# Optimization experiments

Measured on AMD Instinct MI355X. Metric: run time of the kernel, lower is better.

The kernel has to match this reference:

```python
import jax, jax.numpy as jnp
import numpy as np

B, H, L, DK, DV = 8, 8, 1024, 64, 64
N = B * H
TEMP = 8.0  # sqrt(d_k)
A_MIX, B_MIX, C_MIX = 0.1, 0.4, 0.1


def setup_inputs() -> dict:
    key = jax.random.key(0)
    ks = jax.random.split(key, 6)
    q = jax.random.normal(ks[0], (N, L, DK), jnp.float32)
    k = jax.random.normal(ks[1], (N, L, DK), jnp.float32)
    v = jax.random.normal(ks[2], (N, L, DV), jnp.float32)
    q_rm = jax.random.normal(ks[3], (N, L, DK), jnp.float32)
    attn_pre = jax.random.normal(ks[4], (N, L, L), jnp.float32)
    conv_w = jax.random.normal(ks[5], (H, H, 3, 3), jnp.float32) * 0.05  # OIHW, no bias
    # causal mask: True where masked (j > i), broadcast over N
    mask = jnp.broadcast_to(jnp.triu(jnp.ones((L, L), bool), 1), (N, L, L))
    return {"q": q, "k": k, "v": v, "q_rm": q_rm, "attn_pre": attn_pre,
            "conv_w": conv_w, "mask": mask, "fg": 1}


def sift_down_right(src, filled):
    # R[..,1:,1:] = src[..,:-1,:-1]; R[..,0,:] = filled[..,0,:]; R[..,:,0] = filled[..,:,0]
    top = filled[:, 0:1, :]                    # [N,1,L]
    left = filled[:, 1:, 0:1]                  # [N,L-1,1]
    body = jnp.concatenate([left, src[:, :-1, :-1]], axis=-1)  # [N,L-1,L]
    return jnp.concatenate([top, body], axis=1)


def sift_down(src, filled):
    top = filled[:, 0:1, :]
    return jnp.concatenate([top, src[:, :-1, :]], axis=1)


def reference(q, k, v, q_rm, attn_pre, conv_w, mask, fg):
    attn = jnp.einsum('nqd,nkd->nqk', q, k) / TEMP
    attn_rm = jnp.einsum('nqd,nkd->nqk', q_rm, k) / TEMP
    # conv refinement of masked attn_rm, per (batch, head) grid
    x = jnp.where(mask, 0.0, attn_rm).reshape(-1, H, L, L)  # [B,H,L,L]
    x = jax.lax.conv_general_dilated(x, conv_w, (1, 1), 'SAME',
                                     dimension_numbers=('NCHW', 'OIHW', 'NCHW'))
    x = jax.nn.relu(x).reshape(-1, L, L)
    attn_cnn = sift_down_right(x, attn_rm) if fg == 1 else sift_down(x, attn_rm)
    attn_cnn = attn_cnn * C_MIX + attn_rm * (1.0 - C_MIX)
    attn = attn_cnn * B_MIX + attn * (1.0 - B_MIX)
    attn = attn_pre * A_MIX + attn * (1.0 - A_MIX)
    attn = jnp.where(mask, -jnp.inf, attn)
    attn = jax.nn.softmax(attn, axis=-1)
    # dropout is identity in eval/deterministic baseline
    out = jnp.einsum('nqk,nkd->nqd', attn, v)
    return out, attn
```

## Files before the change

### kernel.cpp

```cpp
#include <hip/hip_runtime.h>
#include <cstdint>
#include <cstddef>
#include <math.h>

#define L_ 1024
#define DK_ 64
#define DV_ 64
#define N_ 64
#define H_ 8
#define B_ 8

__device__ __forceinline__ float bcast(float v, int src) {
  return __int_as_float(__builtin_amdgcn_readlane(__float_as_int(v), src));
}

__global__ __launch_bounds__(256) void k1_qk_tril(
    const float* __restrict__ qrm, const float* __restrict__ kk,
    float* __restrict__ xm) {
  const int n  = blockIdx.z;
  const int q0 = blockIdx.y * 64;
  const int j0 = blockIdx.x * 64;
  const int t  = threadIdx.x;

  if (j0 > q0) {
    const float4 z = make_float4(0.f, 0.f, 0.f, 0.f);
    #pragma unroll
    for (int i = 0; i < 4; ++i) {
      const int row = (t >> 4) + i * 16;
      const int c4  = t & 15;
      float4* p = (float4*)(xm + ((size_t)(n * L_ + q0 + row)) * L_ + j0);
      p[c4] = z;
    }
    return;
  }

  __shared__ float As[64][65];
  __shared__ float Bs[64][65];
  #pragma unroll
  for (int i = 0; i < 4; ++i) {
    const int row = (t >> 4) + i * 16;
    const int c4  = t & 15;
    const float4 a = ((const float4*)(qrm + ((size_t)(n * L_ + q0 + row)) * DK_))[c4];
    const float4 b = ((const float4*)(kk  + ((size_t)(n * L_ + j0 + row)) * DK_))[c4];
    As[row][c4 * 4 + 0] = a.x; As[row][c4 * 4 + 1] = a.y;
    As[row][c4 * 4 + 2] = a.z; As[row][c4 * 4 + 3] = a.w;
    Bs[row][c4 * 4 + 0] = b.x; Bs[row][c4 * 4 + 1] = b.y;
    Bs[row][c4 * 4 + 2] = b.z; Bs[row][c4 * 4 + 3] = b.w;
  }
  __syncthreads();

  const int ty = t >> 4, tx = t & 15;
  float acc[4][4];
  #pragma unroll
  for (int i = 0; i < 4; ++i)
    #pragma unroll
    for (int j = 0; j < 4; ++j) acc[i][j] = 0.f;

  for (int d = 0; d < 64; ++d) {
    float a[4], b[4];
    #pragma unroll
    for (int i = 0; i < 4; ++i) a[i] = As[ty * 4 + i][d];
    #pragma unroll
    for (int j = 0; j < 4; ++j) b[j] = Bs[tx * 4 + j][d];
    #pragma unroll
    for (int i = 0; i < 4; ++i)
      #pragma unroll
      for (int j = 0; j < 4; ++j) acc[i][j] += a[i] * b[j];
  }

  #pragma unroll
  for (int i = 0; i < 4; ++i) {
    const int gq = q0 + ty * 4 + i;
    float* rowp = xm + ((size_t)(n * L_ + gq)) * L_;
    #pragma unroll
    for (int j = 0; j < 4; ++j) {
      const int gj = j0 + tx * 4 + j;
      rowp[gj] = (gj <= gq) ? acc[i][j] * 0.125f : 0.f;
    }
  }
}

__global__ __launch_bounds__(256) void k2_conv(
    const float* __restrict__ xm, const float* __restrict__ w,
    float* __restrict__ xs) {
  const int ct = blockIdx.x, rt = blockIdx.y, b = blockIdx.z;
  const int r0 = rt * 4, c0 = ct * 64;
  if (c0 > r0 + 4) return;

  __shared__ float in_s[8][6][68];
  __shared__ float ws[576];
  const int t = threadIdx.x;

  for (int i = t; i < 576; i += 256) ws[i] = w[i];
  for (int e = t; e < 8 * 6 * 66; e += 256) {
    const int hi  = e / 396;
    const int rem = e - hi * 396;
    const int rr  = rem / 66;
    const int cc  = rem - rr * 66;
    const int gr  = r0 - 1 + rr;
    const int gc  = c0 - 1 + cc;
    float v = 0.f;
    if (gr >= 0 && gr < L_ && gc >= 0 && gc < L_)
      v = xm[((size_t)((b * 8 + hi) * L_ + gr)) * L_ + gc];
    in_s[hi][rr][cc] = v;
  }
  __syncthreads();

  const int cc = t & 63;
  const int rr = t >> 6;
  float acc[8];
  #pragma unroll
  for (int ho = 0; ho < 8; ++ho) acc[ho] = 0.f;

  #pragma unroll
  for (int hi = 0; hi < 8; ++hi) {
    float iv[3][3];
    #pragma unroll
    for (int di = 0; di < 3; ++di)
      #pragma unroll
      for (int dj = 0; dj < 3; ++dj)
        iv[di][dj] = in_s[hi][rr + di][cc + dj];
    #pragma unroll
    for (int ho = 0; ho < 8; ++ho) {
      const float* wp = &ws[(ho * 8 + hi) * 9];
      #pragma unroll
      for (int di = 0; di < 3; ++di)
        #pragma unroll
        for (int dj = 0; dj < 3; ++dj)
          acc[ho] += iv[di][dj] * wp[di * 3 + dj];
    }
  }

  const int gr = r0 + rr, gc = c0 + cc;
  #pragma unroll
  for (int ho = 0; ho < 8; ++ho)
    xs[((size_t)((b * 8 + ho) * L_ + gr)) * L_ + gc] = fmaxf(acc[ho], 0.f);
}

__global__ __launch_bounds__(256) void k3_fused(
    const float* __restrict__ q, const float* __restrict__ kk,
    const float* __restrict__ v, const float* __restrict__ pre,
    const int* __restrict__ fgp, const float* __restrict__ xs,
    float* attn, float* __restrict__ out) {
  const int bid  = blockIdx.y * gridDim.x + blockIdx.x;
  const int work = (bid & 7) * 512 + (bid >> 3);
  const int n    = work >> 6;
  const int q0   = (63 - (work & 63)) * 16;

  const int t    = threadIdx.x;
  const int lane = t & 63;
  const int g    = t >> 6;
  const int fg   = *fgp;

  const int srow = t >> 4;
  const int c4   = t & 15;

  __shared__ float tb[2][64][65];

  const float* qb = q + ((size_t)(n * L_ + q0)) * DK_;
  float qreg[4];
  #pragma unroll
  for (int i = 0; i < 4; ++i) qreg[i] = qb[(size_t)(g + i * 4) * DK_ + lane];

  float m[4], l[4];
  #pragma unroll
  for (int i = 0; i < 4; ++i) { m[i] = -INFINITY; l[i] = 0.f; }

  int r_[4];
  #pragma unroll
  for (int i = 0; i < 4; ++i) r_[i] = q0 + g + i * 4;

  const int ntiles = (q0 >> 6) + 1;
  const float* kbase = kk + (size_t)n * L_ * DK_;

  #pragma unroll
  for (int i = 0; i < 4; ++i) {
    const int row = srow + i * 16;
    const float4 kx = *(const float4*)(kbase + (size_t)row * DK_ + c4 * 4);
    tb[0][c4 * 4 + 0][row] = kx.x;
    tb[0][c4 * 4 + 1][row] = kx.y;
    tb[0][c4 * 4 + 2][row] = kx.z;
    tb[0][c4 * 4 + 3][row] = kx.w;
  }
  __syncthreads();

  for (int tile = 0; tile < ntiles; ++tile) {
    const int cur = tile & 1, nxt = cur ^ 1;
    const int j0 = tile * 64;
    const int j  = j0 + lane;
    const bool havenext = (tile + 1) < ntiles;

    float4 kpre[4];
    if (havenext) {
      const float* kb2 = kbase + (size_t)(j0 + 64) * DK_;
      #pragma unroll
      for (int i = 0; i < 4; ++i)
        kpre[i] = *(const float4*)(kb2 + (size_t)(srow + i * 16) * DK_ + c4 * 4);
    }

    float rmv[4], prv[4], xsv[4];
    #pragma unroll
    for (int i = 0; i < 4; ++i) {
      const int r = r_[i];
      const bool act = (j <= r);
      rmv[i] = act ? attn[((size_t)(n * L_ + r)) * L_ + j] : 0.f;
      prv[i] = act ? pre[((size_t)(n * L_ + r)) * L_ + j] : 0.f;
      if (fg == 1)
        xsv[i] = (act && r > 0 && j > 0)
                     ? xs[((size_t)(n * L_ + r - 1)) * L_ + (j - 1)] : 0.f;
      else
        xsv[i] = (act && r > 0)
                     ? xs[((size_t)(n * L_ + r - 1)) * L_ + j] : 0.f;
    }

    float dot[4] = {0.f, 0.f, 0.f, 0.f};
    #pragma unroll
    for (int d = 0; d < 64; ++d) {
      const float kd = tb[cur][d][lane];
      #pragma unroll
      for (int i = 0; i < 4; ++i) dot[i] += bcast(qreg[i], d) * kd;
    }

    #pragma unroll
    for (int i = 0; i < 4; ++i) {
      const int r = r_[i];
      float s = -INFINITY;
      if (j <= r) {
        const float sqk = dot[i] * 0.125f;
        const float cnn = (fg == 1)
                              ? ((r == 0 || j == 0) ? rmv[i] : xsv[i])
                              : ((r == 0) ? rmv[i] : xsv[i]);
        const float mixed = cnn * 0.1f + rmv[i] * 0.9f;
        const float a2    = mixed * 0.4f + sqk * 0.6f;
        s = prv[i] * 0.1f + a2 * 0.9f;
      }
      attn[((size_t)(n * L_ + r)) * L_ + j] = s;

      float mt = s;
      #pragma unroll
      for (int o = 32; o > 0; o >>= 1) mt = fmaxf(mt, __shfl_xor(mt, o));
      const float mn = fmaxf(m[i], mt);
      float es = __expf(s - mn);
      #pragma unroll
      for (int o = 32; o > 0; o >>= 1) es += __shfl_xor(es, o);
      l[i] = l[i] * __expf(m[i] - mn) + es;
      m[i] = mn;
    }

    if (havenext) {
      #pragma unroll
      for (int i = 0; i < 4; ++i) {
        const int row = srow + i * 16;
        tb[nxt][c4 * 4 + 0][row] = kpre[i].x;
        tb[nxt][c4 * 4 + 1][row] = kpre[i].y;
        tb[nxt][c4 * 4 + 2][row] = kpre[i].z;
        tb[nxt][c4 * 4 + 3][row] = kpre[i].w;
      }
    }
    __syncthreads();
  }

  float invl[4];
  #pragma unroll
  for (int i = 0; i < 4; ++i) invl[i] = 1.f / l[i];

  float acc[4] = {0.f, 0.f, 0.f, 0.f};
  const float* vb = v + (size_t)n * L_ * DV_;

  #pragma unroll
  for (int i = 0; i < 4; ++i) {
    const int row = srow + i * 16;
    const float4 vx = *(const float4*)(vb + (size_t)row * DV_ + c4 * 4);
    tb[0][row][c4 * 4 + 0] = vx.x;
    tb[0][row][c4 * 4 + 1] = vx.y;
    tb[0][row][c4 * 4 + 2] = vx.z;
    tb[0][row][c4 * 4 + 3] = vx.w;
  }
  float s_cur[4];
  #pragma unroll
  for (int i = 0; i < 4; ++i)
    s_cur[i] = attn[((size_t)(n * L_ + r_[i])) * L_ + lane];
  __syncthreads();

  for (int tile = 0; tile < ntiles; ++tile) {
    const int cur = tile & 1, nxt = cur ^ 1;
    const int j0 = tile * 64;
    const int j  = j0 + lane;
    const bool havenext = (tile + 1) < ntiles;

    float4 vpre[4];
    float s_nxt[4];
    if (havenext) {
      const float* vb2 = vb + (size_t)(j0 + 64) * DV_;
      #pragma unroll
      for (int i = 0; i < 4; ++i)
        vpre[i] = *(const float4*)(vb2 + (size_t)(srow + i * 16) * DV_ + c4 * 4);
      #pragma unroll
      for (int i = 0; i < 4; ++i)
        s_nxt[i] = attn[((size_t)(n * L_ + r_[i])) * L_ + j + 64];
    }

    float p[4];
    #pragma unroll
    for (int i = 0; i < 4; ++i) {
      p[i] = __expf(s_cur[i] - m[i]) * invl[i];
      attn[((size_t)(n * L_ + r_[i])) * L_ + j] = p[i];
    }

    #pragma unroll
    for (int c = 0; c < 64; ++c) {
      const float vv = tb[cur][c][lane];
      #pragma unroll
      for (int i = 0; i < 4; ++i) acc[i] += bcast(p[i], c) * vv;
    }

    if (havenext) {
      #pragma unroll
      for (int i = 0; i < 4; ++i) {
        const int row = srow + i * 16;
        tb[nxt][row][c4 * 4 + 0] = vpre[i].x;
        tb[nxt][row][c4 * 4 + 1] = vpre[i].y;
        tb[nxt][row][c4 * 4 + 2] = vpre[i].z;
        tb[nxt][row][c4 * 4 + 3] = vpre[i].w;
      }
      #pragma unroll
      for (int i = 0; i < 4; ++i) s_cur[i] = s_nxt[i];
    }
    __syncthreads();
  }

  #pragma unroll
  for (int i = 0; i < 4; ++i)
    out[((size_t)(n * L_ + r_[i])) * DV_ + lane] = acc[i];
}

extern "C" void kernel_launch(void* const* d_in, const int* in_sizes, int n_in,
                              void* d_out, int out_size, void* d_ws,
                              size_t ws_size, hipStream_t stream) {
  const float* q   = (const float*)d_in[0];
  const float* kk  = (const float*)d_in[1];
  const float* v   = (const float*)d_in[2];
  const float* qrm = (const float*)d_in[3];
  const float* pre = (const float*)d_in[4];
  const float* cw  = (const float*)d_in[5];
  const int* fg = (const int*)d_in[7];

  float* out  = (float*)d_out;
  float* attn = out + (size_t)N_ * L_ * DV_;
  float* xs   = (float*)d_ws;

  k1_qk_tril<<<dim3(16, 16, 64), 256, 0, stream>>>(qrm, kk, attn);
  k2_conv<<<dim3(16, 256, 8), 256, 0, stream>>>(attn, cw, xs);
  k3_fused<<<dim3(64, 64), 256, 0, stream>>>(q, kk, v, pre, fg, xs, attn, out);
}
```

Before: 1.620 ms.

## Vectorize shared-memory tiles and defer softmax wave reductions to end

The first kernel pads its LDS tiles to 68 floats, stores and reads them as float4, and reassigns output columns to a strided tx+16*j pattern to cut LDS instruction count and bank conflicts. The fused kernel replaces the per-tile cross-lane max/sum shuffles with per-lane online softmax statistics that are combined once after the loop. It also gives the V tile a padded float4-aligned layout for vectorized stores. The running max now starts at -1e30 instead of -inf so lanes that see only masked entries avoid NaN from inf minus inf. The trade-off is slightly different rounding order in the QK products and the softmax sum.

```diff
diff --git a/kernel.cpp b/kernel.cpp
--- a/kernel.cpp
+++ b/kernel.cpp
@@ -34,18 +34,16 @@
     return;
   }
 
-  __shared__ float As[64][65];
-  __shared__ float Bs[64][65];
+  __shared__ float As[64][68];
+  __shared__ float Bs[64][68];
   #pragma unroll
   for (int i = 0; i < 4; ++i) {
     const int row = (t >> 4) + i * 16;
     const int c4  = t & 15;
     const float4 a = ((const float4*)(qrm + ((size_t)(n * L_ + q0 + row)) * DK_))[c4];
     const float4 b = ((const float4*)(kk  + ((size_t)(n * L_ + j0 + row)) * DK_))[c4];
-    As[row][c4 * 4 + 0] = a.x; As[row][c4 * 4 + 1] = a.y;
-    As[row][c4 * 4 + 2] = a.z; As[row][c4 * 4 + 3] = a.w;
-    Bs[row][c4 * 4 + 0] = b.x; Bs[row][c4 * 4 + 1] = b.y;
-    Bs[row][c4 * 4 + 2] = b.z; Bs[row][c4 * 4 + 3] = b.w;
+    *(float4*)&As[row][c4 * 4] = a;
+    *(float4*)&Bs[row][c4 * 4] = b;
   }
   __syncthreads();
 
@@ -56,16 +54,19 @@
     #pragma unroll
     for (int j = 0; j < 4; ++j) acc[i][j] = 0.f;
 
-  for (int d = 0; d < 64; ++d) {
-    float a[4], b[4];
-    #pragma unroll
-    for (int i = 0; i < 4; ++i) a[i] = As[ty * 4 + i][d];
-    #pragma unroll
-    for (int j = 0; j < 4; ++j) b[j] = Bs[tx * 4 + j][d];
+  #pragma unroll
+  for (int d0 = 0; d0 < 64; d0 += 4) {
+    float4 a4[4], b4[4];
+    #pragma unroll
+    for (int i = 0; i < 4; ++i) a4[i] = *(const float4*)&As[ty * 4 + i][d0];
+    #pragma unroll
+    for (int j = 0; j < 4; ++j) b4[j] = *(const float4*)&Bs[tx + 16 * j][d0];
     #pragma unroll
     for (int i = 0; i < 4; ++i)
       #pragma unroll
-      for (int j = 0; j < 4; ++j) acc[i][j] += a[i] * b[j];
+      for (int j = 0; j < 4; ++j)
+        acc[i][j] += a4[i].x * b4[j].x + a4[i].y * b4[j].y +
+                     a4[i].z * b4[j].z + a4[i].w * b4[j].w;
   }
 
   #pragma unroll
@@ -74,7 +75,7 @@
     float* rowp = xm + ((size_t)(n * L_ + gq)) * L_;
     #pragma unroll
     for (int j = 0; j < 4; ++j) {
-      const int gj = j0 + tx * 4 + j;
+      const int gj = j0 + tx + 16 * j;
       rowp[gj] = (gj <= gq) ? acc[i][j] * 0.125f : 0.f;
     }
   }
@@ -155,7 +156,9 @@
   const int srow = t >> 4;
   const int c4   = t & 15;
 
-  __shared__ float tb[2][64][65];
+  __shared__ float tbraw[8704];
+#define KT(b, d, r) tbraw[(b) * 4160 + (d) * 65 + (r)]
+#define VTP(b, c)   (&tbraw[(b) * 4352 + (c) * 68])
 
   const float* qb = q + ((size_t)(n * L_ + q0)) * DK_;
   float qreg[4];
@@ -164,7 +167,7 @@
 
   float m[4], l[4];
   #pragma unroll
-  for (int i = 0; i < 4; ++i) { m[i] = -INFINITY; l[i] = 0.f; }
+  for (int i = 0; i < 4; ++i) { m[i] = -1e30f; l[i] = 0.f; }
 
   int r_[4];
   #pragma unroll
@@ -177,10 +180,10 @@
   for (int i = 0; i < 4; ++i) {
     const int row = srow + i * 16;
     const float4 kx = *(const float4*)(kbase + (size_t)row * DK_ + c4 * 4);
-    tb[0][c4 * 4 + 0][row] = kx.x;
-    tb[0][c4 * 4 + 1][row] = kx.y;
-    tb[0][c4 * 4 + 2][row] = kx.z;
-    tb[0][c4 * 4 + 3][row] = kx.w;
+    KT(0, c4 * 4 + 0, row) = kx.x;
+    KT(0, c4 * 4 + 1, row) = kx.y;
+    KT(0, c4 * 4 + 2, row) = kx.z;
+    KT(0, c4 * 4 + 3, row) = kx.w;
   }
   __syncthreads();
 
@@ -216,7 +219,7 @@
     float dot[4] = {0.f, 0.f, 0.f, 0.f};
     #pragma unroll
     for (int d = 0; d < 64; ++d) {
-      const float kd = tb[cur][d][lane];
+      const float kd = KT(cur, d, lane);
       #pragma unroll
       for (int i = 0; i < 4; ++i) dot[i] += bcast(qreg[i], d) * kd;
     }
@@ -236,14 +239,8 @@
       }
       attn[((size_t)(n * L_ + r)) * L_ + j] = s;
 
-      float mt = s;
-      #pragma unroll
-      for (int o = 32; o > 0; o >>= 1) mt = fmaxf(mt, __shfl_xor(mt, o));
-      const float mn = fmaxf(m[i], mt);
-      float es = __expf(s - mn);
-      #pragma unroll
-      for (int o = 32; o > 0; o >>= 1) es += __shfl_xor(es, o);
-      l[i] = l[i] * __expf(m[i] - mn) + es;
+      const float mn = fmaxf(m[i], s);
+      l[i] = l[i] * __expf(m[i] - mn) + __expf(s - mn);
       m[i] = mn;
     }
 
@@ -251,13 +248,25 @@
       #pragma unroll
       for (int i = 0; i < 4; ++i) {
         const int row = srow + i * 16;
-        tb[nxt][c4 * 4 + 0][row] = kpre[i].x;
-        tb[nxt][c4 * 4 + 1][row] = kpre[i].y;
-        tb[nxt][c4 * 4 + 2][row] = kpre[i].z;
-        tb[nxt][c4 * 4 + 3][row] = kpre[i].w;
+        KT(nxt, c4 * 4 + 0, row) = kpre[i].x;
+        KT(nxt, c4 * 4 + 1, row) = kpre[i].y;
+        KT(nxt, c4 * 4 + 2, row) = kpre[i].z;
+        KT(nxt, c4 * 4 + 3, row) = kpre[i].w;
       }
     }
     __syncthreads();
+  }
+
+  #pragma unroll
+  for (int i = 0; i < 4; ++i) {
+    float mf = m[i];
+    #pragma unroll
+    for (int o = 32; o > 0; o >>= 1) mf = fmaxf(mf, __shfl_xor(mf, o));
+    float ls = l[i] * __expf(m[i] - mf);
+    #pragma unroll
+    for (int o = 32; o > 0; o >>= 1) ls += __shfl_xor(ls, o);
+    m[i] = mf;
+    l[i] = ls;
   }
 
   float invl[4];
@@ -271,10 +280,7 @@
   for (int i = 0; i < 4; ++i) {
     const int row = srow + i * 16;
     const float4 vx = *(const float4*)(vb + (size_t)row * DV_ + c4 * 4);
-    tb[0][row][c4 * 4 + 0] = vx.x;
-    tb[0][row][c4 * 4 + 1] = vx.y;
-    tb[0][row][c4 * 4 + 2] = vx.z;
-    tb[0][row][c4 * 4 + 3] = vx.w;
+    *(float4*)(VTP(0, row) + c4 * 4) = vx;
   }
   float s_cur[4];
   #pragma unroll
@@ -309,7 +315,7 @@
 
     #pragma unroll
     for (int c = 0; c < 64; ++c) {
-      const float vv = tb[cur][c][lane];
+      const float vv = VTP(cur, c)[lane];
       #pragma unroll
       for (int i = 0; i < 4; ++i) acc[i] += bcast(p[i], c) * vv;
     }
@@ -318,10 +324,7 @@
       #pragma unroll
       for (int i = 0; i < 4; ++i) {
         const int row = srow + i * 16;
-        tb[nxt][row][c4 * 4 + 0] = vpre[i].x;
-        tb[nxt][row][c4 * 4 + 1] = vpre[i].y;
-        tb[nxt][row][c4 * 4 + 2] = vpre[i].z;
-        tb[nxt][row][c4 * 4 + 3] = vpre[i].w;
+        *(float4*)(VTP(nxt, row) + c4 * 4) = vpre[i];
       }
       #pragma unroll
       for (int i = 0; i < 4; ++i) s_cur[i] = s_nxt[i];
@@ -332,6 +335,8 @@
   #pragma unroll
   for (int i = 0; i < 4; ++i)
     out[((size_t)(n * L_ + r_[i])) * DV_ + lane] = acc[i];
+#undef KT
+#undef VTP
 }
 
 extern "C" void kernel_launch(void* const* d_in, const int* in_sizes, int n_in,
```

Measured after the change: 1.862 ms. 1.15x slower.
